# Optimization experiments

Hardware: AMD Instinct MI355X
Metric: run time of the kernel (lower is better)

## Reference

```python
import jax, jax.numpy as jnp
import numpy as np

B, T, V, C = 8, 2048, 50257, 768


def setup_inputs() -> dict:
    key = jax.random.key(0)
    k1, k2 = jax.random.split(key)
    idx = jax.random.randint(k1, (B, T), 0, V)          # (B,T) token ids
    emb = jax.random.normal(k2, (V, C), dtype=jnp.float32)  # embedding table
    return {"idx": idx, "emb": emb}


def _rosa(x):
    """Exact ROSA predictor: longest-suffix-match DP over (B,T,T)."""
    Bx, Tx = x.shape
    eq = (x[:, :, None] == x[:, None, :]).astype(jnp.int32)  # (B,T,T)

    # Sequential diagonal recurrence: L[i,j] = (L[i-1,j-1] + 1) * eq[i,j]
    def step(prev, eq_row):  # prev, eq_row: (B,T)
        cur = (jnp.pad(prev[:, :-1], ((0, 0), (1, 0))) + 1) * eq_row
        return cur, cur

    init = jnp.zeros((Bx, Tx), jnp.int32)  # L[0,:] = 0
    _, rows = jax.lax.scan(step, init, jnp.swapaxes(eq, 0, 1)[1:])  # (T-1,B,T)
    L = jnp.swapaxes(jnp.concatenate([init[None], rows], axis=0), 0, 1)  # (B,T,T)

    mask = jnp.tril(jnp.ones((Tx, Tx), dtype=bool), -1)  # strict lower triangle
    j = jnp.arange(Tx, dtype=jnp.float32)
    TIE = 1e-5  # tie-breaker favoring larger j (matches original)
    scored = jnp.where(mask[None], L.astype(jnp.float32) + j[None, None, :] * TIE, -1.0)
    best_j = jnp.argmax(scored, axis=2)                     # (B,T)
    pred_idx = jnp.minimum(best_j + 1, Tx - 1)
    preds = jnp.take_along_axis(x, pred_idx, axis=1)        # (B,T)
    no_match = jnp.max(jnp.where(mask[None], L, 0), axis=2) == 0
    return jnp.where(no_match, -1, preds)


def reference(idx, emb):
    p = _rosa(idx)                        # (B,T) predicted ids, -1 = no match
    out = emb[jnp.clip(p, 0)]             # (B,T,C)
    return jnp.where((p == -1)[..., None], 0.0, out)
```

## Files before the change

### kernel.cpp

```cpp
#include <hip/hip_runtime.h>

#define BATCH 8
#define TLEN  2048
#define CDIM  768

__global__ __launch_bounds__(256) void rosa_pred_kernel(const int* __restrict__ idx,
                                                        int* __restrict__ pred) {
    __shared__ int xs[TLEN];
    const int b   = blockIdx.x;
    const int i0  = blockIdx.y * 64;
    const int tid = threadIdx.x;

    const int* __restrict__ xrow = idx + b * TLEN;
    for (int t = tid; t < TLEN; t += 256) xs[t] = xrow[t];
    __syncthreads();

    const int i    = i0 + (tid >> 2);
    const int part = tid & 3;
    const int xi   = xs[i];

    const int chunk = (i + 3) >> 2;
    const int jlo   = part * chunk;
    const int jhi   = min(jlo + chunk, i);

    float bestS = -1.0f;
    int   bestJ = 0;

    for (int j = jlo; j < jhi; ++j) {
        if (xs[j] == xi) {
            int L = 1;
            int m = 1;
            while (m <= j && xs[i - m] == xs[j - m]) { ++L; ++m; }
            const float s = __fadd_rn((float)L, __fmul_rn((float)j, 1e-5f));
            if (s > bestS) { bestS = s; bestJ = j; }
        }
    }

    #pragma unroll
    for (int off = 1; off < 4; off <<= 1) {
        const float oS = __shfl_xor(bestS, off, 64);
        const int   oJ = __shfl_xor(bestJ, off, 64);
        if (oS > bestS || (oS == bestS && oJ < bestJ)) { bestS = oS; bestJ = oJ; }
    }

    if (part == 0) {
        int p = -1;
        if (bestS >= 0.5f) {
            const int pi = min(bestJ + 1, TLEN - 1);
            p = xs[pi];
        }
        pred[b * TLEN + i] = p;
    }
}

__global__ __launch_bounds__(256) void rosa_gather_kernel(const int* __restrict__ pred,
                                                          const float* __restrict__ emb,
                                                          float* __restrict__ out) {
    const int row  = blockIdx.x * 4 + (threadIdx.x >> 6);
    const int lane = threadIdx.x & 63;
    const int p    = pred[row];

    float4* __restrict__ o = (float4*)(out + (size_t)row * CDIM);
    if (p < 0) {
        const float4 z = make_float4(0.f, 0.f, 0.f, 0.f);
        #pragma unroll
        for (int k = 0; k < 3; ++k) o[lane + k * 64] = z;
    } else {
        const float4* __restrict__ e = (const float4*)(emb + (size_t)p * CDIM);
        #pragma unroll
        for (int k = 0; k < 3; ++k) o[lane + k * 64] = e[lane + k * 64];
    }
}

extern "C" void kernel_launch(void* const* d_in, const int* in_sizes, int n_in,
                              void* d_out, int out_size, void* d_ws, size_t ws_size,
                              hipStream_t stream) {
    const int*   idx = (const int*)d_in[0];
    const float* emb = (const float*)d_in[1];
    float*       out = (float*)d_out;
    int*         pred = (int*)d_ws;

    dim3 g1(BATCH, TLEN / 64);
    rosa_pred_kernel<<<g1, 256, 0, stream>>>(idx, pred);

    const int nrows = BATCH * TLEN;
    rosa_gather_kernel<<<nrows / 4, 256, 0, stream>>>(pred, emb, out);
}
```

Before: 234.0 us.

## Fuse ROSA prediction and embedding gather into one wave-per-row kernel

Merges the prediction and gather kernels into one launch, so each wavefront owns one query row: its 64 lanes scan candidate j positions in a strided pattern, reduce the best match with a full-wave shuffle, then write the embedding row directly. This drops the intermediate pred buffer and the second launch, and spreads the triangular j-scan over 64 lanes instead of 4, which reduces per-thread serial work and load imbalance. In exchange, each block reloads the whole 2048-token row into shared memory for only 4 rows, and there are many more blocks.

```diff
diff --git a/kernel.cpp b/kernel.cpp
--- a/kernel.cpp
+++ b/kernel.cpp
@@ -4,29 +4,30 @@
 #define TLEN  2048
 #define CDIM  768
 
-__global__ __launch_bounds__(256) void rosa_pred_kernel(const int* __restrict__ idx,
-                                                        int* __restrict__ pred) {
+__global__ __launch_bounds__(256) void rosa_fused_kernel(const int* __restrict__ idx,
+                                                         const float* __restrict__ emb,
+                                                         float* __restrict__ out) {
     __shared__ int xs[TLEN];
-    const int b   = blockIdx.x;
-    const int i0  = blockIdx.y * 64;
-    const int tid = threadIdx.x;
+    const int b    = blockIdx.y;
+    const int i0   = blockIdx.x * 4;
+    const int tid  = threadIdx.x;
+    const int wave = tid >> 6;
+    const int lane = tid & 63;
 
-    const int* __restrict__ xrow = idx + b * TLEN;
-    for (int t = tid; t < TLEN; t += 256) xs[t] = xrow[t];
+    const int4* __restrict__ xr4 = (const int4*)(idx + b * TLEN);
+    int4* xs4 = (int4*)xs;
+    #pragma unroll
+    for (int t = tid; t < TLEN / 4; t += 256) xs4[t] = xr4[t];
     __syncthreads();
 
-    const int i    = i0 + (tid >> 2);
-    const int part = tid & 3;
-    const int xi   = xs[i];
-
-    const int chunk = (i + 3) >> 2;
-    const int jlo   = part * chunk;
-    const int jhi   = min(jlo + chunk, i);
+    const int i  = i0 + wave;
+    const int xi = xs[i];
 
     float bestS = -1.0f;
     int   bestJ = 0;
 
-    for (int j = jlo; j < jhi; ++j) {
+    #pragma unroll 4
+    for (int j = lane; j < i; j += 64) {
         if (xs[j] == xi) {
             int L = 1;
             int m = 1;
@@ -37,30 +38,15 @@
     }
 
     #pragma unroll
-    for (int off = 1; off < 4; off <<= 1) {
+    for (int off = 32; off >= 1; off >>= 1) {
         const float oS = __shfl_xor(bestS, off, 64);
         const int   oJ = __shfl_xor(bestJ, off, 64);
         if (oS > bestS || (oS == bestS && oJ < bestJ)) { bestS = oS; bestJ = oJ; }
     }
 
-    if (part == 0) {
-        int p = -1;
-        if (bestS >= 0.5f) {
-            const int pi = min(bestJ + 1, TLEN - 1);
-            p = xs[pi];
-        }
-        pred[b * TLEN + i] = p;
-    }
-}
+    const int p = (bestS >= 0.5f) ? xs[min(bestJ + 1, TLEN - 1)] : -1;
 
-__global__ __launch_bounds__(256) void rosa_gather_kernel(const int* __restrict__ pred,
-                                                          const float* __restrict__ emb,
-                                                          float* __restrict__ out) {
-    const int row  = blockIdx.x * 4 + (threadIdx.x >> 6);
-    const int lane = threadIdx.x & 63;
-    const int p    = pred[row];
-
-    float4* __restrict__ o = (float4*)(out + (size_t)row * CDIM);
+    float4* __restrict__ o = (float4*)(out + (size_t)(b * TLEN + i) * CDIM);
     if (p < 0) {
         const float4 z = make_float4(0.f, 0.f, 0.f, 0.f);
         #pragma unroll
@@ -78,11 +64,7 @@
     const int*   idx = (const int*)d_in[0];
     const float* emb = (const float*)d_in[1];
     float*       out = (float*)d_out;
-    int*         pred = (int*)d_ws;
 
-    dim3 g1(BATCH, TLEN / 64);
-    rosa_pred_kernel<<<g1, 256, 0, stream>>>(idx, pred);
-
-    const int nrows = BATCH * TLEN;
-    rosa_gather_kernel<<<nrows / 4, 256, 0, stream>>>(pred, emb, out);
+    dim3 grid(TLEN / 4, BATCH);
+    rosa_fused_kernel<<<grid, 256, 0, stream>>>(idx, emb, out);
 }
```

Result: faster. 200.6 us (-14.3%).
